# Performance work log

Measured on AMD Instinct MI355X. Metric: run time of the kernel, lower is better.

The kernel has to match this reference:

```python
import jax, jax.numpy as jnp
import numpy as np

C = 512
HSIZE = C // 4
D, H, W = 18, 24, 24
N = D * H * W


def setup_inputs() -> dict:
    key = jax.random.key(0)
    ks = jax.random.split(key, 6)
    features = jax.random.normal(ks[0], (1, C, D, H, W), dtype=jnp.float32)
    Wi = jax.random.normal(ks[1], (HSIZE, C), dtype=jnp.float32) * 0.02
    bi = jax.random.normal(ks[2], (HSIZE,), dtype=jnp.float32) * 0.02
    Wj = jax.random.normal(ks[3], (HSIZE, C), dtype=jnp.float32) * 0.02
    bj = jax.random.normal(ks[4], (HSIZE,), dtype=jnp.float32) * 0.02
    # attention_agregate: shape (head=1, 1), xavier-uniform in the original
    agg = jax.random.uniform(ks[5], (1, 1), dtype=jnp.float32, minval=-1.0, maxval=1.0)
    return {"features": features, "Wi": Wi, "bi": bi, "Wj": Wj, "bj": bj, "agg": agg}


def reference(features, Wi, bi, Wj, bj, agg):
    # features: [1, C, D, H, W]; 1x1x1 convs == channel-wise matmuls
    x = features.reshape(C, N)                      # [C, N]
    fi = (Wi @ x + bi[:, None]).T                   # [N, hsize]  (conv_i output, permuted)
    fj = Wj @ x + bj[:, None]                       # [hsize, N]  (conv_j output)
    fk = x.T                                        # [N, C]      (raw features, NOT conv_k)
    # original: attn = (fi @ fj) * agg / N ; out = attn @ fk
    # linear chain reassociated: fi @ (fj @ fk) * agg / N  (same math, no NxN intermediate)
    scale = agg[0, 0] / jnp.float32(N)
    out_flat = (fi @ (fj @ fk)) * scale             # [N, C]
    return features + out_flat.T.reshape(1, C, D, H, W)
```

## Files before the change

kernel.cpp:

```cpp
#include <hip/hip_runtime.h>
#include <hip/hip_bf16.h>

#define C_   512
#define HS   128
#define NN   10368

typedef __bf16 bf16x8 __attribute__((ext_vector_type(8)));
typedef __bf16 bf16x2 __attribute__((ext_vector_type(2)));
typedef float  f32x4  __attribute__((ext_vector_type(4)));

__device__ __forceinline__ bf16x8 load_f32x8_as_bf16(const float* __restrict__ p) {
    float4 v0 = *(const float4*)p;
    float4 v1 = *(const float4*)(p + 4);
    bf16x8 o;
    o[0] = (__bf16)v0.x; o[1] = (__bf16)v0.y; o[2] = (__bf16)v0.z; o[3] = (__bf16)v0.w;
    o[4] = (__bf16)v1.x; o[5] = (__bf16)v1.y; o[6] = (__bf16)v1.z; o[7] = (__bf16)v1.w;
    return o;
}

__global__ __launch_bounds__(512, 2)
void k_fused12(const float* __restrict__ feat,
               const float* __restrict__ Wi, const float* __restrict__ Wj,
               const float* __restrict__ bi, const float* __restrict__ bj,
               __bf16* __restrict__ xb, __bf16* __restrict__ fj,
               __bf16* __restrict__ finm, float* __restrict__ Mtf) {
    const int b = blockIdx.x;
    const int t = threadIdx.x;
    if (b >= 324) {
        const int z = b - 324;
        f32x4 zv = {0.f, 0.f, 0.f, 0.f};
        float* p = Mtf + z * 4096 + t * 8;
        *(f32x4*)(p) = zv; *(f32x4*)(p + 4) = zv;
        return;
    }
    __shared__ __bf16 xt[32][520];
    const int n0 = b * 32;
    {
        const int tn = t & 31;
        const int c2 = (t >> 5) * 2;
        float va[16], vb[16];
        #pragma unroll
        for (int p = 0; p < 16; p++) {
            const int c = p * 32 + c2;
            va[p] = feat[(size_t)c * NN + n0 + tn];
            vb[p] = feat[(size_t)(c + 1) * NN + n0 + tn];
        }
        #pragma unroll
        for (int p = 0; p < 16; p++) {
            const int c = p * 32 + c2;
            __bf16 b0 = (__bf16)va[p], b1 = (__bf16)vb[p];
            xb[(size_t)c * NN + n0 + tn]       = b0;
            xb[(size_t)(c + 1) * NN + n0 + tn] = b1;
            bf16x2 pk; pk[0] = b0; pk[1] = b1;
            *(bf16x2*)&xt[tn][c] = pk;
        }
    }
    __syncthreads();
    const int w    = t >> 6;
    const int lane = t & 63;
    const int l16  = lane & 15;
    const int q    = lane >> 4;
    const int h0   = w * 16;
    f32x4 afj[2] = {};
    f32x4 afi[2] = {};
    #pragma unroll 4
    for (int k = 0; k < 512; k += 32) {
        bf16x8 ln0 = *(const bf16x8*)&xt[l16][k + q * 8];
        bf16x8 ln1 = *(const bf16x8*)&xt[16 + l16][k + q * 8];
        bf16x8 wjf = load_f32x8_as_bf16(Wj + (h0 + l16) * 512 + k + q * 8);
        bf16x8 wif = load_f32x8_as_bf16(Wi + (h0 + l16) * 512 + k + q * 8);
        afj[0] = __builtin_amdgcn_mfma_f32_16x16x32_bf16(wjf, ln0, afj[0], 0, 0, 0);
        afj[1] = __builtin_amdgcn_mfma_f32_16x16x32_bf16(wjf, ln1, afj[1], 0, 0, 0);
        afi[0] = __builtin_amdgcn_mfma_f32_16x16x32_bf16(ln0, wif, afi[0], 0, 0, 0);
        afi[1] = __builtin_amdgcn_mfma_f32_16x16x32_bf16(ln1, wif, afi[1], 0, 0, 0);
    }
    const float4 bjv = *(const float4*)(bj + h0 + q * 4);
    const float  biv = bi[h0 + l16];
    #pragma unroll
    for (int tt = 0; tt < 2; tt++)
        #pragma unroll
        for (int r = 0; r < 4; r++) {
            const int h = h0 + q * 4 + r;
            const int n = n0 + 16 * tt + l16;
            fj[(size_t)h * NN + n] = (__bf16)(afj[tt][r] + (&bjv.x)[r]);
        }
    #pragma unroll
    for (int i2 = 0; i2 < 2; i2++)
        #pragma unroll
        for (int r = 0; r < 4; r++) {
            const int n = n0 + 16 * i2 + q * 4 + r;
            const int h = h0 + l16;
            finm[(size_t)n * HS + h] = (__bf16)(afi[i2][r] + biv);
        }
}

__global__ __launch_bounds__(512, 2)
void k_gemm3(const __bf16* __restrict__ xb, const __bf16* __restrict__ fj,
             float* __restrict__ Mtf) {
    __shared__ float red[8][64][17];
    const int b    = blockIdx.x;
    const int t    = threadIdx.x;
    const int v    = t >> 6;
    const int lane = t & 63;
    const int l16  = lane & 15;
    const int q    = lane >> 4;
    const int tile = b & 63, g = b >> 6;
    const int c0 = (tile >> 2) * 32, h0 = (tile & 3) * 32;
    const int chunk = g * 8 + v;
    const int s0 = (chunk * 324) >> 6;
    const int s1 = ((chunk + 1) * 324) >> 6;
    f32x4 acc[2][2] = {};
    bf16x8 a[2], bb[2];
    {
        const int k = s0 * 32;
        a[0]  = *(const bf16x8*)(xb + (size_t)(c0 + l16) * NN + k + q * 8);
        a[1]  = *(const bf16x8*)(xb + (size_t)(c0 + 16 + l16) * NN + k + q * 8);
        bb[0] = *(const bf16x8*)(fj + (size_t)(h0 + l16) * NN + k + q * 8);
        bb[1] = *(const bf16x8*)(fj + (size_t)(h0 + 16 + l16) * NN + k + q * 8);
    }
    for (int s = s0; s < s1 - 1; s++) {
        const int kn = (s + 1) * 32;
        bf16x8 a2[2], b2[2];
        a2[0] = *(const bf16x8*)(xb + (size_t)(c0 + l16) * NN + kn + q * 8);
        a2[1] = *(const bf16x8*)(xb + (size_t)(c0 + 16 + l16) * NN + kn + q * 8);
        b2[0] = *(const bf16x8*)(fj + (size_t)(h0 + l16) * NN + kn + q * 8);
        b2[1] = *(const bf16x8*)(fj + (size_t)(h0 + 16 + l16) * NN + kn + q * 8);
        #pragma unroll
        for (int i = 0; i < 2; i++)
            #pragma unroll
            for (int tt = 0; tt < 2; tt++)
                acc[i][tt] = __builtin_amdgcn_mfma_f32_16x16x32_bf16(a[i], bb[tt], acc[i][tt], 0, 0, 0);
        a[0] = a2[0]; a[1] = a2[1]; bb[0] = b2[0]; bb[1] = b2[1];
    }
    #pragma unroll
    for (int i = 0; i < 2; i++)
        #pragma unroll
        for (int tt = 0; tt < 2; tt++)
            acc[i][tt] = __builtin_amdgcn_mfma_f32_16x16x32_bf16(a[i], bb[tt], acc[i][tt], 0, 0, 0);
    #pragma unroll
    for (int i = 0; i < 2; i++)
        #pragma unroll
        for (int tt = 0; tt < 2; tt++)
            #pragma unroll
            for (int r = 0; r < 4; r++)
                red[v][lane][i * 8 + tt * 4 + r] = acc[i][tt][r];
    __syncthreads();
    #pragma unroll
    for (int u = 0; u < 2; u++) {
        const int idx = t * 2 + u;
        const int lane_e = idx >> 4, j = idx & 15;
        float s = 0.f;
        #pragma unroll
        for (int vv = 0; vv < 8; vv++) s += red[vv][lane_e][j];
        const int i = j >> 3, tt = (j >> 2) & 1, r = j & 3;
        const int qe = lane_e >> 4, le = lane_e & 15;
        const int c = c0 + 16 * i + qe * 4 + r;
        const int h = h0 + 16 * tt + le;
        atomicAdd(&Mtf[c * HS + h], s);
    }
}

__global__ __launch_bounds__(256, 2)
void k_gemm4(const float* __restrict__ Mtf, const __bf16* __restrict__ finm,
             const float* __restrict__ feat, const float* __restrict__ agg,
             float* __restrict__ out) {
    const int w    = blockIdx.x * 4 + (threadIdx.x >> 6);
    const int lane = threadIdx.x & 63;
    const int l16  = lane & 15;
    const int q    = lane >> 4;
    const int c0 = (w & 15) * 32, n0 = (w >> 4) * 32;
    const float scale = agg[0] * (1.0f / (float)NN);
    f32x4 acc[2][2] = {};
    #pragma unroll
    for (int k = 0; k < 128; k += 32) {
        bf16x8 a[2], b[2];
        #pragma unroll
        for (int i = 0; i < 2; i++)
            a[i] = load_f32x8_as_bf16(Mtf + (c0 + 16 * i + l16) * HS + k + q * 8);
        #pragma unroll
        for (int tt = 0; tt < 2; tt++)
            b[tt] = *(const bf16x8*)(finm + (size_t)(n0 + 16 * tt + l16) * HS + k + q * 8);
        #pragma unroll
        for (int i = 0; i < 2; i++)
            #pragma unroll
            for (int tt = 0; tt < 2; tt++)
                acc[i][tt] = __builtin_amdgcn_mfma_f32_16x16x32_bf16(a[i], b[tt], acc[i][tt], 0, 0, 0);
    }
    float fv[2][2][4];
    #pragma unroll
    for (int i = 0; i < 2; i++)
        #pragma unroll
        for (int tt = 0; tt < 2; tt++)
            #pragma unroll
            for (int r = 0; r < 4; r++) {
                const int c = c0 + 16 * i + q * 4 + r;
                const int n = n0 + 16 * tt + l16;
                fv[i][tt][r] = feat[(size_t)c * NN + n];
            }
    #pragma unroll
    for (int i = 0; i < 2; i++)
        #pragma unroll
        for (int tt = 0; tt < 2; tt++)
            #pragma unroll
            for (int r = 0; r < 4; r++) {
                const int c = c0 + 16 * i + q * 4 + r;
                const int n = n0 + 16 * tt + l16;
                out[(size_t)c * NN + n] = fv[i][tt][r] + scale * acc[i][tt][r];
            }
}

extern "C" void kernel_launch(void* const* d_in, const int* in_sizes, int n_in,
                              void* d_out, int out_size, void* d_ws, size_t ws_size,
                              hipStream_t stream) {
    const float* feat = (const float*)d_in[0];
    const float* Wi   = (const float*)d_in[1];
    const float* bi   = (const float*)d_in[2];
    const float* Wj   = (const float*)d_in[3];
    const float* bj   = (const float*)d_in[4];
    const float* agg  = (const float*)d_in[5];
    float* out = (float*)d_out;

    char* ws = (char*)d_ws;
    __bf16* xb   = (__bf16*)(ws);
    __bf16* fj   = (__bf16*)(ws + 10616832);
    __bf16* finm = (__bf16*)(ws + 13271040);
    float*  Mtf  = (float*) (ws + 15925248);

    k_fused12<<<340,  512, 0, stream>>>(feat, Wi, Wj, bi, bj, xb, fj, finm, Mtf);
    k_gemm3 <<<512,  512, 0, stream>>>(xb, fj, Mtf);
    k_gemm4 <<<1296, 256, 0, stream>>>(Mtf, finm, feat, agg, out);
}
```

Measured before the change: 142.3 us.

## Fuse three kernels into one cooperative persistent kernel with grid syncs

Merges the projection, the reduction GEMM and the output GEMM into one cooperative kernel that separates its phases with grid-wide syncs, removing two kernel launch boundaries and their tails. It also stops writing the bf16 copy of the features: the reduction phase reads the fp32 features directly and converts them on the fly. The weights are converted to bf16 once up front instead of in every tile. The trade-offs are grid.sync overhead, a grid capped at 512 blocks that loops over tiles, and a higher occupancy target that may pressure registers.

```diff
diff --git a/kernel.cpp b/kernel.cpp
--- a/kernel.cpp
+++ b/kernel.cpp
@@ -1,11 +1,15 @@
 #include <hip/hip_runtime.h>
 #include <hip/hip_bf16.h>
+#include <hip/hip_cooperative_groups.h>
+
+namespace cg = cooperative_groups;
 
 #define C_   512
 #define HS   128
 #define NN   10368
 
 typedef __bf16 bf16x8 __attribute__((ext_vector_type(8)));
+typedef __bf16 bf16x4 __attribute__((ext_vector_type(4)));
 typedef __bf16 bf16x2 __attribute__((ext_vector_type(2)));
 typedef float  f32x4  __attribute__((ext_vector_type(4)));
 
@@ -18,195 +22,186 @@
     return o;
 }
 
-__global__ __launch_bounds__(512, 2)
-void k_fused12(const float* __restrict__ feat,
-               const float* __restrict__ Wi, const float* __restrict__ Wj,
-               const float* __restrict__ bi, const float* __restrict__ bj,
-               __bf16* __restrict__ xb, __bf16* __restrict__ fj,
-               __bf16* __restrict__ finm, float* __restrict__ Mtf) {
-    const int b = blockIdx.x;
-    const int t = threadIdx.x;
-    if (b >= 324) {
-        const int z = b - 324;
-        f32x4 zv = {0.f, 0.f, 0.f, 0.f};
-        float* p = Mtf + z * 4096 + t * 8;
-        *(f32x4*)(p) = zv; *(f32x4*)(p + 4) = zv;
-        return;
-    }
-    __shared__ __bf16 xt[32][520];
-    const int n0 = b * 32;
-    {
-        const int tn = t & 31;
-        const int c2 = (t >> 5) * 2;
-        float va[16], vb[16];
-        #pragma unroll
-        for (int p = 0; p < 16; p++) {
-            const int c = p * 32 + c2;
-            va[p] = feat[(size_t)c * NN + n0 + tn];
-            vb[p] = feat[(size_t)(c + 1) * NN + n0 + tn];
-        }
-        #pragma unroll
-        for (int p = 0; p < 16; p++) {
-            const int c = p * 32 + c2;
-            __bf16 b0 = (__bf16)va[p], b1 = (__bf16)vb[p];
-            xb[(size_t)c * NN + n0 + tn]       = b0;
-            xb[(size_t)(c + 1) * NN + n0 + tn] = b1;
-            bf16x2 pk; pk[0] = b0; pk[1] = b1;
-            *(bf16x2*)&xt[tn][c] = pk;
-        }
-    }
-    __syncthreads();
-    const int w    = t >> 6;
+__global__ __launch_bounds__(512, 4)
+void k_all(const float* __restrict__ feat,
+           const float* __restrict__ Wi, const float* __restrict__ Wj,
+           const float* __restrict__ bi, const float* __restrict__ bj,
+           const float* __restrict__ agg,
+           __bf16* __restrict__ Wib, __bf16* __restrict__ Wjb,
+           __bf16* __restrict__ fj, __bf16* __restrict__ finm,
+           float* __restrict__ Mtf, float* __restrict__ out) {
+    cg::grid_group grid = cg::this_grid();
+    const int t    = threadIdx.x;
+    const int nb   = gridDim.x;
+    const int gid  = blockIdx.x * 512 + t;
+    const int nthr = nb * 512;
     const int lane = t & 63;
     const int l16  = lane & 15;
     const int q    = lane >> 4;
-    const int h0   = w * 16;
-    f32x4 afj[2] = {};
-    f32x4 afi[2] = {};
-    #pragma unroll 4
-    for (int k = 0; k < 512; k += 32) {
-        bf16x8 ln0 = *(const bf16x8*)&xt[l16][k + q * 8];
-        bf16x8 ln1 = *(const bf16x8*)&xt[16 + l16][k + q * 8];
-        bf16x8 wjf = load_f32x8_as_bf16(Wj + (h0 + l16) * 512 + k + q * 8);
-        bf16x8 wif = load_f32x8_as_bf16(Wi + (h0 + l16) * 512 + k + q * 8);
-        afj[0] = __builtin_amdgcn_mfma_f32_16x16x32_bf16(wjf, ln0, afj[0], 0, 0, 0);
-        afj[1] = __builtin_amdgcn_mfma_f32_16x16x32_bf16(wjf, ln1, afj[1], 0, 0, 0);
-        afi[0] = __builtin_amdgcn_mfma_f32_16x16x32_bf16(ln0, wif, afi[0], 0, 0, 0);
-        afi[1] = __builtin_amdgcn_mfma_f32_16x16x32_bf16(ln1, wif, afi[1], 0, 0, 0);
-    }
-    const float4 bjv = *(const float4*)(bj + h0 + q * 4);
-    const float  biv = bi[h0 + l16];
-    #pragma unroll
-    for (int tt = 0; tt < 2; tt++)
-        #pragma unroll
-        for (int r = 0; r < 4; r++) {
-            const int h = h0 + q * 4 + r;
-            const int n = n0 + 16 * tt + l16;
-            fj[(size_t)h * NN + n] = (__bf16)(afj[tt][r] + (&bjv.x)[r]);
-        }
-    #pragma unroll
-    for (int i2 = 0; i2 < 2; i2++)
-        #pragma unroll
-        for (int r = 0; r < 4; r++) {
-            const int n = n0 + 16 * i2 + q * 4 + r;
-            const int h = h0 + l16;
-            finm[(size_t)n * HS + h] = (__bf16)(afi[i2][r] + biv);
-        }
-}
-
-__global__ __launch_bounds__(512, 2)
-void k_gemm3(const __bf16* __restrict__ xb, const __bf16* __restrict__ fj,
-             float* __restrict__ Mtf) {
-    __shared__ float red[8][64][17];
-    const int b    = blockIdx.x;
-    const int t    = threadIdx.x;
-    const int v    = t >> 6;
-    const int lane = t & 63;
-    const int l16  = lane & 15;
-    const int q    = lane >> 4;
-    const int tile = b & 63, g = b >> 6;
-    const int c0 = (tile >> 2) * 32, h0 = (tile & 3) * 32;
-    const int chunk = g * 8 + v;
-    const int s0 = (chunk * 324) >> 6;
-    const int s1 = ((chunk + 1) * 324) >> 6;
-    f32x4 acc[2][2] = {};
-    bf16x8 a[2], bb[2];
-    {
-        const int k = s0 * 32;
-        a[0]  = *(const bf16x8*)(xb + (size_t)(c0 + l16) * NN + k + q * 8);
-        a[1]  = *(const bf16x8*)(xb + (size_t)(c0 + 16 + l16) * NN + k + q * 8);
-        bb[0] = *(const bf16x8*)(fj + (size_t)(h0 + l16) * NN + k + q * 8);
-        bb[1] = *(const bf16x8*)(fj + (size_t)(h0 + 16 + l16) * NN + k + q * 8);
-    }
-    for (int s = s0; s < s1 - 1; s++) {
-        const int kn = (s + 1) * 32;
-        bf16x8 a2[2], b2[2];
-        a2[0] = *(const bf16x8*)(xb + (size_t)(c0 + l16) * NN + kn + q * 8);
-        a2[1] = *(const bf16x8*)(xb + (size_t)(c0 + 16 + l16) * NN + kn + q * 8);
-        b2[0] = *(const bf16x8*)(fj + (size_t)(h0 + l16) * NN + kn + q * 8);
-        b2[1] = *(const bf16x8*)(fj + (size_t)(h0 + 16 + l16) * NN + kn + q * 8);
+    const int w    = t >> 6;
+
+    __shared__ __align__(16) char shraw[34816];
+    __bf16 (*xt)[520]     = (__bf16(*)[520])shraw;
+    float  (*red)[64][17] = (float(*)[64][17])shraw;
+
+    for (int j4 = gid * 4; j4 < 131072; j4 += nthr * 4) {
+        const float* src; __bf16* dst; int idx;
+        if (j4 < 65536) { src = Wj; dst = Wjb; idx = j4; }
+        else            { src = Wi; dst = Wib; idx = j4 - 65536; }
+        float4 v = *(const float4*)(src + idx);
+        bf16x4 o;
+        o[0] = (__bf16)v.x; o[1] = (__bf16)v.y; o[2] = (__bf16)v.z; o[3] = (__bf16)v.w;
+        *(bf16x4*)(dst + idx) = o;
+    }
+    for (int j = gid * 4; j < 65536; j += nthr * 4) {
+        f32x4 z = {0.f, 0.f, 0.f, 0.f};
+        *(f32x4*)(Mtf + j) = z;
+    }
+    __threadfence();
+    grid.sync();
+
+    for (int tile = blockIdx.x; tile < 324; tile += nb) {
+        const int n0 = tile * 32;
+        __syncthreads();
+        {
+            const int tn = t & 31;
+            const int c2 = (t >> 5) * 2;
+            #pragma unroll
+            for (int p = 0; p < 16; p++) {
+                const int c = p * 32 + c2;
+                float v0 = feat[(size_t)c * NN + n0 + tn];
+                float v1 = feat[(size_t)(c + 1) * NN + n0 + tn];
+                bf16x2 pk; pk[0] = (__bf16)v0; pk[1] = (__bf16)v1;
+                *(bf16x2*)&xt[tn][c] = pk;
+            }
+        }
+        __syncthreads();
+        const int h0 = w * 16;
+        f32x4 afj[2] = {};
+        f32x4 afi[2] = {};
+        #pragma unroll 4
+        for (int k = 0; k < 512; k += 32) {
+            bf16x8 ln0 = *(const bf16x8*)&xt[l16][k + q * 8];
+            bf16x8 ln1 = *(const bf16x8*)&xt[16 + l16][k + q * 8];
+            bf16x8 wjf = *(const bf16x8*)&Wjb[(size_t)(h0 + l16) * C_ + k + q * 8];
+            bf16x8 wif = *(const bf16x8*)&Wib[(size_t)(h0 + l16) * C_ + k + q * 8];
+            afj[0] = __builtin_amdgcn_mfma_f32_16x16x32_bf16(wjf, ln0, afj[0], 0, 0, 0);
+            afj[1] = __builtin_amdgcn_mfma_f32_16x16x32_bf16(wjf, ln1, afj[1], 0, 0, 0);
+            afi[0] = __builtin_amdgcn_mfma_f32_16x16x32_bf16(ln0, wif, afi[0], 0, 0, 0);
+            afi[1] = __builtin_amdgcn_mfma_f32_16x16x32_bf16(ln1, wif, afi[1], 0, 0, 0);
+        }
+        const float4 bjv = *(const float4*)(bj + h0 + q * 4);
+        const float  biv = bi[h0 + l16];
+        #pragma unroll
+        for (int tt = 0; tt < 2; tt++)
+            #pragma unroll
+            for (int r = 0; r < 4; r++) {
+                const int h = h0 + q * 4 + r;
+                const int n = n0 + 16 * tt + l16;
+                fj[(size_t)h * NN + n] = (__bf16)(afj[tt][r] + (&bjv.x)[r]);
+            }
+        #pragma unroll
+        for (int i2 = 0; i2 < 2; i2++)
+            #pragma unroll
+            for (int r = 0; r < 4; r++) {
+                const int n = n0 + 16 * i2 + q * 4 + r;
+                const int h = h0 + l16;
+                finm[(size_t)n * HS + h] = (__bf16)(afi[i2][r] + biv);
+            }
+    }
+    __threadfence();
+    grid.sync();
+
+    for (int bu = blockIdx.x; bu < 512; bu += nb) {
+        const int vv    = t >> 6;
+        const int tile2 = bu & 63, g = bu >> 6;
+        const int c0 = (tile2 >> 2) * 32, hb = (tile2 & 3) * 32;
+        const int chunk = g * 8 + vv;
+        const int s0 = (chunk * 324) >> 6;
+        const int s1 = ((chunk + 1) * 324) >> 6;
+        f32x4 acc[2][2] = {};
+        for (int s = s0; s < s1; s++) {
+            const int k = s * 32;
+            bf16x8 a[2], bb[2];
+            a[0]  = load_f32x8_as_bf16(feat + (size_t)(c0 + l16) * NN + k + q * 8);
+            a[1]  = load_f32x8_as_bf16(feat + (size_t)(c0 + 16 + l16) * NN + k + q * 8);
+            bb[0] = *(const bf16x8*)(fj + (size_t)(hb + l16) * NN + k + q * 8);
+            bb[1] = *(const bf16x8*)(fj + (size_t)(hb + 16 + l16) * NN + k + q * 8);
+            #pragma unroll
+            for (int i = 0; i < 2; i++)
+                #pragma unroll
+                for (int tt = 0; tt < 2; tt++)
+                    acc[i][tt] = __builtin_amdgcn_mfma_f32_16x16x32_bf16(a[i], bb[tt], acc[i][tt], 0, 0, 0);
+        }
+        __syncthreads();
         #pragma unroll
         for (int i = 0; i < 2; i++)
             #pragma unroll
             for (int tt = 0; tt < 2; tt++)
-                acc[i][tt] = __builtin_amdgcn_mfma_f32_16x16x32_bf16(a[i], bb[tt], acc[i][tt], 0, 0, 0);
-        a[0] = a2[0]; a[1] = a2[1]; bb[0] = b2[0]; bb[1] = b2[1];
-    }
-    #pragma unroll
-    for (int i = 0; i < 2; i++)
-        #pragma unroll
-        for (int tt = 0; tt < 2; tt++)
-            acc[i][tt] = __builtin_amdgcn_mfma_f32_16x16x32_bf16(a[i], bb[tt], acc[i][tt], 0, 0, 0);
-    #pragma unroll
-    for (int i = 0; i < 2; i++)
-        #pragma unroll
-        for (int tt = 0; tt < 2; tt++)
-            #pragma unroll
-            for (int r = 0; r < 4; r++)
-                red[v][lane][i * 8 + tt * 4 + r] = acc[i][tt][r];
-    __syncthreads();
-    #pragma unroll
-    for (int u = 0; u < 2; u++) {
-        const int idx = t * 2 + u;
-        const int lane_e = idx >> 4, j = idx & 15;
-        float s = 0.f;
-        #pragma unroll
-        for (int vv = 0; vv < 8; vv++) s += red[vv][lane_e][j];
-        const int i = j >> 3, tt = (j >> 2) & 1, r = j & 3;
-        const int qe = lane_e >> 4, le = lane_e & 15;
-        const int c = c0 + 16 * i + qe * 4 + r;
-        const int h = h0 + 16 * tt + le;
-        atomicAdd(&Mtf[c * HS + h], s);
-    }
-}
-
-__global__ __launch_bounds__(256, 2)
-void k_gemm4(const float* __restrict__ Mtf, const __bf16* __restrict__ finm,
-             const float* __restrict__ feat, const float* __restrict__ agg,
-             float* __restrict__ out) {
-    const int w    = blockIdx.x * 4 + (threadIdx.x >> 6);
-    const int lane = threadIdx.x & 63;
-    const int l16  = lane & 15;
-    const int q    = lane >> 4;
-    const int c0 = (w & 15) * 32, n0 = (w >> 4) * 32;
+                #pragma unroll
+                for (int r = 0; r < 4; r++)
+                    red[vv][lane][i * 8 + tt * 4 + r] = acc[i][tt][r];
+        __syncthreads();
+        #pragma unroll
+        for (int u = 0; u < 2; u++) {
+            const int idx = t * 2 + u;
+            const int lane_e = idx >> 4, j = idx & 15;
+            float s = 0.f;
+            #pragma unroll
+            for (int z = 0; z < 8; z++) s += red[z][lane_e][j];
+            const int i = j >> 3, tt = (j >> 2) & 1, r = j & 3;
+            const int qe = lane_e >> 4, le = lane_e & 15;
+            const int c = c0 + 16 * i + qe * 4 + r;
+            const int h = hb + 16 * tt + le;
+            atomicAdd(&Mtf[c * HS + h], s);
+        }
+    }
+    __threadfence();
+    grid.sync();
+
+    const int gw = gid >> 6;
+    const int nw = nthr >> 6;
     const float scale = agg[0] * (1.0f / (float)NN);
-    f32x4 acc[2][2] = {};
-    #pragma unroll
-    for (int k = 0; k < 128; k += 32) {
-        bf16x8 a[2], b[2];
+    for (int u = gw; u < 5184; u += nw) {
+        const int c0 = (u & 15) * 32, n0 = (u >> 4) * 32;
+        f32x4 acc[2][2] = {};
+        #pragma unroll
+        for (int k = 0; k < 128; k += 32) {
+            bf16x8 a[2], b[2];
+            #pragma unroll
+            for (int i = 0; i < 2; i++)
+                a[i] = load_f32x8_as_bf16(Mtf + (c0 + 16 * i + l16) * HS + k + q * 8);
+            #pragma unroll
+            for (int tt = 0; tt < 2; tt++)
+                b[tt] = *(const bf16x8*)(finm + (size_t)(n0 + 16 * tt + l16) * HS + k + q * 8);
+            #pragma unroll
+            for (int i = 0; i < 2; i++)
+                #pragma unroll
+                for (int tt = 0; tt < 2; tt++)
+                    acc[i][tt] = __builtin_amdgcn_mfma_f32_16x16x32_bf16(a[i], b[tt], acc[i][tt], 0, 0, 0);
+        }
+        float fv[2][2][4];
         #pragma unroll
         for (int i = 0; i < 2; i++)
-            a[i] = load_f32x8_as_bf16(Mtf + (c0 + 16 * i + l16) * HS + k + q * 8);
-        #pragma unroll
-        for (int tt = 0; tt < 2; tt++)
-            b[tt] = *(const bf16x8*)(finm + (size_t)(n0 + 16 * tt + l16) * HS + k + q * 8);
+            #pragma unroll
+            for (int tt = 0; tt < 2; tt++)
+                #pragma unroll
+                for (int r = 0; r < 4; r++) {
+                    const int c = c0 + 16 * i + q * 4 + r;
+                    const int n = n0 + 16 * tt + l16;
+                    fv[i][tt][r] = feat[(size_t)c * NN + n];
+                }
         #pragma unroll
         for (int i = 0; i < 2; i++)
             #pragma unroll
             for (int tt = 0; tt < 2; tt++)
-                acc[i][tt] = __builtin_amdgcn_mfma_f32_16x16x32_bf16(a[i], b[tt], acc[i][tt], 0, 0, 0);
-    }
-    float fv[2][2][4];
-    #pragma unroll
-    for (int i = 0; i < 2; i++)
-        #pragma unroll
-        for (int tt = 0; tt < 2; tt++)
-            #pragma unroll
-            for (int r = 0; r < 4; r++) {
-                const int c = c0 + 16 * i + q * 4 + r;
-                const int n = n0 + 16 * tt + l16;
-                fv[i][tt][r] = feat[(size_t)c * NN + n];
-            }
-    #pragma unroll
-    for (int i = 0; i < 2; i++)
-        #pragma unroll
-        for (int tt = 0; tt < 2; tt++)
-            #pragma unroll
-            for (int r = 0; r < 4; r++) {
-                const int c = c0 + 16 * i + q * 4 + r;
-                const int n = n0 + 16 * tt + l16;
-                out[(size_t)c * NN + n] = fv[i][tt][r] + scale * acc[i][tt][r];
-            }
+                #pragma unroll
+                for (int r = 0; r < 4; r++) {
+                    const int c = c0 + 16 * i + q * 4 + r;
+                    const int n = n0 + 16 * tt + l16;
+                    out[(size_t)c * NN + n] = fv[i][tt][r] + scale * acc[i][tt][r];
+                }
+    }
 }
 
 extern "C" void kernel_launch(void* const* d_in, const int* in_sizes, int n_in,
@@ -221,12 +216,24 @@
     float* out = (float*)d_out;
 
     char* ws = (char*)d_ws;
-    __bf16* xb   = (__bf16*)(ws);
-    __bf16* fj   = (__bf16*)(ws + 10616832);
-    __bf16* finm = (__bf16*)(ws + 13271040);
-    float*  Mtf  = (float*) (ws + 15925248);
-
-    k_fused12<<<340,  512, 0, stream>>>(feat, Wi, Wj, bi, bj, xb, fj, finm, Mtf);
-    k_gemm3 <<<512,  512, 0, stream>>>(xb, fj, Mtf);
-    k_gemm4 <<<1296, 256, 0, stream>>>(Mtf, finm, feat, agg, out);
+    __bf16* fj   = (__bf16*)(ws);
+    __bf16* finm = (__bf16*)(ws + 2654208);
+    float*  Mtf  = (float*) (ws + 5308416);
+    __bf16* Wjb  = (__bf16*)(ws + 5570560);
+    __bf16* Wib  = (__bf16*)(ws + 5701632);
+
+    static int nblk = 0;
+    if (nblk == 0) {
+        int per_cu = 0;
+        hipError_t e = hipOccupancyMaxActiveBlocksPerMultiprocessor(
+            &per_cu, reinterpret_cast<const void*>(k_all), 512, 0);
+        nblk = (e == hipSuccess && per_cu >= 1) ? per_cu * 256 : 256;
+        if (nblk > 512) nblk = 512;
+    }
+
+    void* args[] = {(void*)&feat, (void*)&Wi, (void*)&Wj, (void*)&bi, (void*)&bj,
+                    (void*)&agg, (void*)&Wib, (void*)&Wjb, (void*)&fj, (void*)&finm,
+                    (void*)&Mtf, (void*)&out};
+    hipLaunchCooperativeKernel(reinterpret_cast<const void*>(k_all),
+                               dim3(nblk), dim3(512), args, 0, stream);
 }
```

New measurement: 357.0 us. 151% more time.
